# Kernel tuning notes

Measured on AMD Instinct MI355X. Metric: run time of the kernel, lower is better.

The kernel has to match this reference:

```python
import jax, jax.numpy as jnp
import numpy as np

N_NODES = 50000
N_EDGES = 1600000
N_GRAPHS = 64
D = 128


def setup_inputs() -> dict:
    key = jax.random.key(0)
    ks = jax.random.split(key, 6)
    x = jax.random.normal(ks[0], (N_NODES, D), dtype=jnp.float32)
    W1 = jax.random.normal(ks[1], (D, D), dtype=jnp.float32) * (1.0 / np.sqrt(D))
    b1 = jnp.zeros((D,), dtype=jnp.float32)
    W2 = jax.random.normal(ks[2], (D, D), dtype=jnp.float32) * (1.0 / np.sqrt(D))
    b2 = jnp.zeros((D,), dtype=jnp.float32)
    edge_index = jax.random.randint(ks[3], (2, N_EDGES), 0, N_NODES, dtype=jnp.int64)
    batch = jnp.sort(jax.random.randint(ks[4], (N_NODES,), 0, N_GRAPHS, dtype=jnp.int64))
    return {"x": x, "W1": W1, "b1": b1, "W2": W2, "b2": b2,
            "edge_index": edge_index, "batch": batch}


def _gcn_conv(x, W, b, src, dst, coef, n_nodes):
    # GCNConv: h = W^T x; out_i = sum_{j->i} norm_ij * h_j + b
    h = x @ W                                  # [N, D_out]
    msg = h[src] * coef[:, None]               # [E+N, D_out] gather + scale
    out = jax.ops.segment_sum(msg, dst, num_segments=n_nodes)
    return out + b


def reference(x, W1, b1, W2, b2, edge_index, batch):
    n_nodes = x.shape[0]
    # add self-loops (PyG GCNConv default add_self_loops=True)
    loop = jnp.arange(n_nodes, dtype=edge_index.dtype)
    src = jnp.concatenate([edge_index[0], loop])
    dst = jnp.concatenate([edge_index[1], loop])
    # symmetric normalization: deg counted on target side incl. self-loops
    deg = jax.ops.segment_sum(jnp.ones_like(dst, dtype=x.dtype), dst,
                              num_segments=n_nodes)
    dinv = jnp.where(deg > 0, jax.lax.rsqrt(deg), 0.0)
    coef = dinv[src] * dinv[dst]               # [E+N]

    h = jax.nn.relu(_gcn_conv(x, W1, b1, src, dst, coef, n_nodes))
    h = jax.nn.relu(_gcn_conv(h, W2, b2, src, dst, coef, n_nodes))

    # global_mean_pool over batch ids
    sums = jax.ops.segment_sum(h, batch, num_segments=N_GRAPHS)
    cnts = jax.ops.segment_sum(jnp.ones((n_nodes,), dtype=h.dtype), batch,
                               num_segments=N_GRAPHS)
    return sums / jnp.maximum(cnts, 1.0)[:, None]
```

## Files before the change

kernel.cpp:

```cpp
#include <hip/hip_runtime.h>
#include <stdint.h>

#define DF 128
#define PAD 80
#define BCAP 8192
#define CCAP 96
#define PCHUNK 16

typedef __attribute__((ext_vector_type(8))) __bf16 bf16x8;
typedef __attribute__((ext_vector_type(4))) float f32x4;

__device__ inline unsigned bf16rn(float x) {
    unsigned u = __float_as_uint(x);
    return (u + 0x7FFFu + ((u >> 16) & 1u)) >> 16;
}
__device__ inline float4 unpack_bf16x4(uint2 v) {
    float4 r;
    r.x = __uint_as_float(v.x << 16);
    r.y = __uint_as_float(v.x & 0xFFFF0000u);
    r.z = __uint_as_float(v.y << 16);
    r.w = __uint_as_float(v.y & 0xFFFF0000u);
    return r;
}
__device__ inline void addf4(float4& a, float4 f) {
    a.x += f.x; a.y += f.y; a.z += f.z; a.w += f.w;
}

__global__ __launch_bounds__(256) void bucket_sp(const int* __restrict__ src,
        const int* __restrict__ dst, unsigned* __restrict__ buckets,
        int* __restrict__ cnts, int E, int nchunk, int nbuck) {
    __shared__ int loc[256];
    int tid = threadIdx.x;
    loc[tid] = 0;
    __syncthreads();
    int chunk = blockIdx.x;
    int beg = chunk * BCAP;
    int end = beg + BCAP; if (end > E) end = E;
    for (int i = beg + tid; i < end; i += 256) {
        int d = dst[i];
        int s = src[i];
        int b = d >> 8;
        int slot = atomicAdd(&loc[b], 1);
        if (slot < CCAP)
            buckets[((size_t)b * nchunk + chunk) * CCAP + slot] =
                ((unsigned)(d & 255) << 16) | (unsigned)s;
    }
    __syncthreads();
    for (int b = tid; b < nbuck; b += 256) {
        int c = loc[b]; if (c > CCAP) c = CCAP;
        cnts[(size_t)b * nchunk + chunk] = c;
    }
}

__global__ __launch_bounds__(256) void csr_sp(const unsigned* __restrict__ buckets,
        const int* __restrict__ cnts, unsigned short* __restrict__ csr,
        int* __restrict__ cnt, float* __restrict__ dinv,
        const int* __restrict__ batch, int* __restrict__ gse,
        int N, int G, int nchunk) {
    __shared__ int nodecnt[256];
    int tid = threadIdx.x;
    nodecnt[tid] = 0;
    __syncthreads();
    int b = blockIdx.x;
    const unsigned* __restrict__ bk = buckets + (size_t)b * nchunk * CCAP;
    const int* __restrict__ cr = cnts + (size_t)b * nchunk;
    for (int c = tid; c < nchunk; c += 256) {
        int nb = cr[c];
        const unsigned* __restrict__ cell = bk + (size_t)c * CCAP;
        for (int i = 0; i < nb; ++i) {
            unsigned w = cell[i];
            int dl = w >> 16;
            int r = atomicAdd(&nodecnt[dl], 1);
            if (r < PAD)
                csr[(size_t)(b * 256 + dl) * PAD + r] = (unsigned short)(w & 0xFFFFu);
        }
    }
    __syncthreads();
    int node = b * 256 + tid;
    if (node < N) {
        int c = nodecnt[tid];
        cnt[node] = c;
        dinv[node] = rsqrtf((float)(c + 1));
        int bg = batch[node];
        if (node == 0 || batch[node - 1] != bg) gse[bg] = node;
        if (node == N - 1 || batch[node + 1] != bg) gse[G + bg] = node + 1;
    }
}

__global__ __launch_bounds__(256) void gemm_mfma(
    const float* __restrict__ A, const float* __restrict__ W,
    const float* __restrict__ dinv, uint2* __restrict__ g2, int N)
{
    __shared__ unsigned short Wt[128 * 136];
    int tid = threadIdx.x;
    int wv = tid >> 6;
    int l  = tid & 63;
    int lr = l & 15;
    int lk = (l >> 4) * 8;
    int r  = blockIdx.x * 64 + wv * 16 + lr;
    int rc = (r < N) ? r : (N - 1);

    float4 areg[8];
    const float* Arow = A + (size_t)rc * DF;
    #pragma unroll
    for (int ks = 0; ks < 4; ++ks) {
        areg[2 * ks]     = *(const float4*)(Arow + ks * 32 + lk);
        areg[2 * ks + 1] = *(const float4*)(Arow + ks * 32 + lk + 4);
    }

    #pragma unroll
    for (int i = 0; i < 16; ++i) {
        int flat = i * 256 + tid;
        int k = flat >> 5;
        int c4 = (flat & 31) << 2;
        float4 w4 = *(const float4*)(W + (size_t)k * DF + c4);
        Wt[(c4 + 0) * 136 + k] = (unsigned short)bf16rn(w4.x);
        Wt[(c4 + 1) * 136 + k] = (unsigned short)bf16rn(w4.y);
        Wt[(c4 + 2) * 136 + k] = (unsigned short)bf16rn(w4.z);
        Wt[(c4 + 3) * 136 + k] = (unsigned short)bf16rn(w4.w);
    }

    union U8 { unsigned short s[8]; bf16x8 v; };
    bf16x8 aH[4], aL[4];
    #pragma unroll
    for (int ks = 0; ks < 4; ++ks) {
        U8 uh, ul;
        const float* f0 = (const float*)&areg[2 * ks];
        #pragma unroll
        for (int j = 0; j < 8; ++j) {
            float a = f0[j];
            unsigned hb = bf16rn(a);
            float hf = __uint_as_float(hb << 16);
            uh.s[j] = (unsigned short)hb;
            ul.s[j] = (unsigned short)bf16rn(a - hf);
        }
        aH[ks] = uh.v; aL[ks] = ul.v;
    }

    __syncthreads();

    f32x4 zero = {0.f, 0.f, 0.f, 0.f};
    f32x4 acc[8];
    #pragma unroll
    for (int t = 0; t < 8; ++t) acc[t] = zero;

    #pragma unroll
    for (int ks = 0; ks < 4; ++ks) {
        int ko = ks * 32 + lk;
        #pragma unroll
        for (int t = 0; t < 8; ++t) {
            bf16x8 wf = *(const bf16x8*)&Wt[(t * 16 + lr) * 136 + ko];
            acc[t] = __builtin_amdgcn_mfma_f32_16x16x32_bf16(wf, aH[ks], acc[t], 0, 0, 0);
            acc[t] = __builtin_amdgcn_mfma_f32_16x16x32_bf16(wf, aL[ks], acc[t], 0, 0, 0);
        }
    }

    if (r < N) {
        float di = dinv[r];
        int hi4 = l >> 4;
        #pragma unroll
        for (int t = 0; t < 8; ++t) {
            unsigned lo = bf16rn(di * acc[t][0]) | (bf16rn(di * acc[t][1]) << 16);
            unsigned hi = bf16rn(di * acc[t][2]) | (bf16rn(di * acc[t][3]) << 16);
            uint2 o; o.x = lo; o.y = hi;
            g2[(size_t)r * 32 + t * 4 + hi4] = o;
        }
    }
}

__global__ __launch_bounds__(256) void agg_kernel(
    const uint2* __restrict__ g, const unsigned short* __restrict__ csr,
    const int* __restrict__ cnt, const float* __restrict__ dinv,
    const float* __restrict__ bias, float* __restrict__ out, int n)
{
    int idx = blockIdx.x * 256 + threadIdx.x;
    int node = idx >> 5;
    int lane = threadIdx.x & 31;
    if (node >= n) return;
    int deg = cnt[node]; if (deg > PAD) deg = PAD;
    const unsigned short* __restrict__ row = csr + (size_t)node * PAD;

    float4 a0 = unpack_bf16x4(g[(size_t)node * 32 + lane]);
    float4 a1 = {0.f, 0.f, 0.f, 0.f};
    float4 a2 = {0.f, 0.f, 0.f, 0.f};
    float4 a3 = {0.f, 0.f, 0.f, 0.f};

    int e = 0;
    for (; e + 7 < deg; e += 8) {
        uint4 w = *(const uint4*)(row + e);
        int s0 = (int)(w.x & 0xFFFFu), s1 = (int)(w.x >> 16);
        int s2 = (int)(w.y & 0xFFFFu), s3 = (int)(w.y >> 16);
        int s4 = (int)(w.z & 0xFFFFu), s5 = (int)(w.z >> 16);
        int s6 = (int)(w.w & 0xFFFFu), s7 = (int)(w.w >> 16);
        uint2 v0 = g[(size_t)s0 * 32 + lane];
        uint2 v1 = g[(size_t)s1 * 32 + lane];
        uint2 v2 = g[(size_t)s2 * 32 + lane];
        uint2 v3 = g[(size_t)s3 * 32 + lane];
        uint2 v4 = g[(size_t)s4 * 32 + lane];
        uint2 v5 = g[(size_t)s5 * 32 + lane];
        uint2 v6 = g[(size_t)s6 * 32 + lane];
        uint2 v7 = g[(size_t)s7 * 32 + lane];
        addf4(a0, unpack_bf16x4(v0)); addf4(a1, unpack_bf16x4(v1));
        addf4(a2, unpack_bf16x4(v2)); addf4(a3, unpack_bf16x4(v3));
        addf4(a0, unpack_bf16x4(v4)); addf4(a1, unpack_bf16x4(v5));
        addf4(a2, unpack_bf16x4(v6)); addf4(a3, unpack_bf16x4(v7));
    }
    for (; e + 3 < deg; e += 4) {
        int s0 = row[e], s1 = row[e + 1], s2 = row[e + 2], s3 = row[e + 3];
        uint2 v0 = g[(size_t)s0 * 32 + lane];
        uint2 v1 = g[(size_t)s1 * 32 + lane];
        uint2 v2 = g[(size_t)s2 * 32 + lane];
        uint2 v3 = g[(size_t)s3 * 32 + lane];
        addf4(a0, unpack_bf16x4(v0)); addf4(a1, unpack_bf16x4(v1));
        addf4(a2, unpack_bf16x4(v2)); addf4(a3, unpack_bf16x4(v3));
    }
    for (; e < deg; ++e) {
        uint2 v = g[(size_t)row[e] * 32 + lane];
        addf4(a0, unpack_bf16x4(v));
    }
    float sx = (a0.x + a1.x) + (a2.x + a3.x);
    float sy = (a0.y + a1.y) + (a2.y + a3.y);
    float sz = (a0.z + a1.z) + (a2.z + a3.z);
    float sw = (a0.w + a1.w) + (a2.w + a3.w);

    float di = dinv[node];
    float4 b4 = ((const float4*)bias)[lane];
    float4 o;
    o.x = fmaxf(fmaf(di, sx, b4.x), 0.f);
    o.y = fmaxf(fmaf(di, sy, b4.y), 0.f);
    o.z = fmaxf(fmaf(di, sz, b4.z), 0.f);
    o.w = fmaxf(fmaf(di, sw, b4.w), 0.f);
    ((float4*)out)[(size_t)node * 32 + lane] = o;
}

__global__ __launch_bounds__(256) void pool_partial(
    const float* __restrict__ h, const int* __restrict__ gse,
    float* __restrict__ acc, int G)
{
    __shared__ float part[256];
    int gi = blockIdx.x >> 4;
    int ck = blockIdx.x & (PCHUNK - 1);
    int s = gse[gi], e = gse[G + gi];
    int len = e - s;
    if (len <= 0) return;
    int per = (len + PCHUNK - 1) / PCHUNK;
    int r0 = s + ck * per;
    int r1 = r0 + per; if (r1 > e) r1 = e;
    int c = threadIdx.x & 127;
    int rr = threadIdx.x >> 7;
    float sum = 0.f;
    for (int r = r0 + rr; r < r1; r += 2) sum += h[(size_t)r * DF + c];
    part[threadIdx.x] = sum;
    __syncthreads();
    if (threadIdx.x < 128) {
        float t = part[threadIdx.x] + part[threadIdx.x + 128];
        atomicAdd(&acc[gi * DF + c], t);
    }
}

__global__ __launch_bounds__(128) void pool_final(
    const float* __restrict__ acc, const int* __restrict__ gse,
    float* __restrict__ out, int G)
{
    int gi = blockIdx.x;
    int c = threadIdx.x;
    int s = gse[gi], e = gse[G + gi];
    out[gi * DF + c] = (e > s) ? (acc[gi * DF + c] / (float)(e - s)) : 0.f;
}

static inline char* align256(char* p) {
    return (char*)(((uintptr_t)p + 255) & ~(uintptr_t)255);
}

extern "C" void kernel_launch(void* const* d_in, const int* in_sizes, int n_in,
                              void* d_out, int out_size, void* d_ws, size_t ws_size,
                              hipStream_t stream)
{
    const float* x     = (const float*)d_in[0];
    const float* W1    = (const float*)d_in[1];
    const float* b1    = (const float*)d_in[2];
    const float* W2    = (const float*)d_in[3];
    const float* b2    = (const float*)d_in[4];
    const int*   ei    = (const int*)d_in[5];
    const int*   batch = (const int*)d_in[6];

    int N = in_sizes[0] / DF;
    int E = in_sizes[5] / 2;
    int G = out_size / DF;
    const int* src = ei;
    const int* dst = ei + E;

    int nbuck  = (N + 255) >> 8;
    int nchunk = (E + BCAP - 1) / BCAP;

    char* p = (char*)d_ws;
    p = align256(p);
    int* gse     = (int*)p; p += (size_t)2 * G * 4;
    float* acc   = (float*)p; p += (size_t)G * DF * 4;
    p = align256(p);
    int* cnt     = (int*)p; p += (size_t)N * 4;
    p = align256(p);
    float* dinv  = (float*)p; p += (size_t)N * 4;
    p = align256(p);
    int* cnts    = (int*)p; p += (size_t)nbuck * nchunk * 4;
    p = align256(p);
    unsigned* buckets = (unsigned*)p; p += (size_t)nbuck * nchunk * CCAP * 4;
    p = align256(p);
    unsigned short* csr = (unsigned short*)p; p += (size_t)N * PAD * 2;
    p = align256(p);
    uint2* g2 = (uint2*)p; p += (size_t)N * DF * 2;
    p = align256(p);
    float* h  = (float*)p; p += (size_t)N * DF * 4;

    hipMemsetAsync(gse, 0, (size_t)(2 * G + G * DF) * 4, stream);

    const int thr = 256;

    bucket_sp<<<nchunk, thr, 0, stream>>>(src, dst, buckets, cnts, E, nchunk, nbuck);
    csr_sp<<<nbuck, thr, 0, stream>>>(buckets, cnts, csr, cnt, dinv, batch, gse, N, G, nchunk);

    int gemm_grid = (N + 63) / 64;
    int agg_grid  = (N * 32 + 255) / 256;

    gemm_mfma<<<gemm_grid, thr, 0, stream>>>(x, W1, dinv, g2, N);
    agg_kernel<<<agg_grid, thr, 0, stream>>>(g2, csr, cnt, dinv, b1, h, N);
    gemm_mfma<<<gemm_grid, thr, 0, stream>>>(h, W2, dinv, g2, N);
    agg_kernel<<<agg_grid, thr, 0, stream>>>(g2, csr, cnt, dinv, b2, h, N);
    pool_partial<<<G * PCHUNK, thr, 0, stream>>>(h, gse, acc, G);
    pool_final<<<G, 128, 0, stream>>>(acc, gse, (float*)d_out, G);
}
```

Measured before the change: 208.6 us.

## Split aggregation feature dimension into two column halves across adjacent blocks

```diff
diff --git a/kernel.cpp b/kernel.cpp
--- a/kernel.cpp
+++ b/kernel.cpp
@@ -173,14 +173,16 @@
     const int* __restrict__ cnt, const float* __restrict__ dinv,
     const float* __restrict__ bias, float* __restrict__ out, int n)
 {
-    int idx = blockIdx.x * 256 + threadIdx.x;
-    int node = idx >> 5;
-    int lane = threadIdx.x & 31;
+    int bid = blockIdx.x;
+    int chunk = bid & 1;
+    int node = (bid >> 1) * 16 + (threadIdx.x >> 4);
+    int lane = threadIdx.x & 15;
     if (node >= n) return;
     int deg = cnt[node]; if (deg > PAD) deg = PAD;
     const unsigned short* __restrict__ row = csr + (size_t)node * PAD;
-
-    float4 a0 = unpack_bf16x4(g[(size_t)node * 32 + lane]);
+    int co = chunk * 16 + lane;
+
+    float4 a0 = unpack_bf16x4(g[(size_t)node * 32 + co]);
     float4 a1 = {0.f, 0.f, 0.f, 0.f};
     float4 a2 = {0.f, 0.f, 0.f, 0.f};
     float4 a3 = {0.f, 0.f, 0.f, 0.f};
@@ -192,14 +194,14 @@
         int s2 = (int)(w.y & 0xFFFFu), s3 = (int)(w.y >> 16);
         int s4 = (int)(w.z & 0xFFFFu), s5 = (int)(w.z >> 16);
         int s6 = (int)(w.w & 0xFFFFu), s7 = (int)(w.w >> 16);
-        uint2 v0 = g[(size_t)s0 * 32 + lane];
-        uint2 v1 = g[(size_t)s1 * 32 + lane];
-        uint2 v2 = g[(size_t)s2 * 32 + lane];
-        uint2 v3 = g[(size_t)s3 * 32 + lane];
-        uint2 v4 = g[(size_t)s4 * 32 + lane];
-        uint2 v5 = g[(size_t)s5 * 32 + lane];
-        uint2 v6 = g[(size_t)s6 * 32 + lane];
-        uint2 v7 = g[(size_t)s7 * 32 + lane];
+        uint2 v0 = g[(size_t)s0 * 32 + co];
+        uint2 v1 = g[(size_t)s1 * 32 + co];
+        uint2 v2 = g[(size_t)s2 * 32 + co];
+        uint2 v3 = g[(size_t)s3 * 32 + co];
+        uint2 v4 = g[(size_t)s4 * 32 + co];
+        uint2 v5 = g[(size_t)s5 * 32 + co];
+        uint2 v6 = g[(size_t)s6 * 32 + co];
+        uint2 v7 = g[(size_t)s7 * 32 + co];
         addf4(a0, unpack_bf16x4(v0)); addf4(a1, unpack_bf16x4(v1));
         addf4(a2, unpack_bf16x4(v2)); addf4(a3, unpack_bf16x4(v3));
         addf4(a0, unpack_bf16x4(v4)); addf4(a1, unpack_bf16x4(v5));
@@ -207,15 +209,15 @@
     }
     for (; e + 3 < deg; e += 4) {
         int s0 = row[e], s1 = row[e + 1], s2 = row[e + 2], s3 = row[e + 3];
-        uint2 v0 = g[(size_t)s0 * 32 + lane];
-        uint2 v1 = g[(size_t)s1 * 32 + lane];
-        uint2 v2 = g[(size_t)s2 * 32 + lane];
-        uint2 v3 = g[(size_t)s3 * 32 + lane];
+        uint2 v0 = g[(size_t)s0 * 32 + co];
+        uint2 v1 = g[(size_t)s1 * 32 + co];
+        uint2 v2 = g[(size_t)s2 * 32 + co];
+        uint2 v3 = g[(size_t)s3 * 32 + co];
         addf4(a0, unpack_bf16x4(v0)); addf4(a1, unpack_bf16x4(v1));
         addf4(a2, unpack_bf16x4(v2)); addf4(a3, unpack_bf16x4(v3));
     }
     for (; e < deg; ++e) {
-        uint2 v = g[(size_t)row[e] * 32 + lane];
+        uint2 v = g[(size_t)row[e] * 32 + co];
         addf4(a0, unpack_bf16x4(v));
     }
     float sx = (a0.x + a1.x) + (a2.x + a3.x);
@@ -224,13 +226,13 @@
     float sw = (a0.w + a1.w) + (a2.w + a3.w);
 
     float di = dinv[node];
-    float4 b4 = ((const float4*)bias)[lane];
+    float4 b4 = ((const float4*)bias)[co];
     float4 o;
     o.x = fmaxf(fmaf(di, sx, b4.x), 0.f);
     o.y = fmaxf(fmaf(di, sy, b4.y), 0.f);
     o.z = fmaxf(fmaf(di, sz, b4.z), 0.f);
     o.w = fmaxf(fmaf(di, sw, b4.w), 0.f);
-    ((float4*)out)[(size_t)node * 32 + lane] = o;
+    ((float4*)out)[(size_t)node * 32 + co] = o;
 }
 
 __global__ __launch_bounds__(256) void pool_partial(
@@ -320,7 +322,7 @@
     csr_sp<<<nbuck, thr, 0, stream>>>(buckets, cnts, csr, cnt, dinv, batch, gse, N, G, nchunk);
 
     int gemm_grid = (N + 63) / 64;
-    int agg_grid  = (N * 32 + 255) / 256;
+    int agg_grid  = ((N + 15) / 16) * 2;
 
     gemm_mfma<<<gemm_grid, thr, 0, stream>>>(x, W1, dinv, g2, N);
     agg_kernel<<<agg_grid, thr, 0, stream>>>(g2, csr, cnt, dinv, b1, h, N);
```

Result: faster. 194.8 us (-6.6%).
